# Kernel optimization log

Measured on AMD Instinct MI355X. Metric: run time of the kernel, lower is better.

## Reference

```python
import jax, jax.numpy as jnp
import numpy as np
import math

B, S, H = 2, 4096, 512
NUM_HEADS = 8
HEAD_DIM = H // NUM_HEADS
RECENCY_DECAY = 0.9


def setup_inputs() -> dict:
    key = jax.random.key(0)
    k1, k2, k3 = jax.random.split(key, 3)
    scale = 1.0 / math.sqrt(H)
    x = jax.random.normal(k1, (B, S, H), dtype=jnp.float32)
    w_qkv = jax.random.normal(k2, (3 * H, H), dtype=jnp.float32) * scale
    w_out = jax.random.normal(k3, (H, H), dtype=jnp.float32) * scale
    b_out = jnp.zeros((H,), dtype=jnp.float32)
    return {"x": x, "w_qkv": w_qkv, "w_out": w_out, "b_out": b_out}


def reference(x, w_qkv, w_out, b_out):
    batch, seq_len, hidden = x.shape
    nh, hd = NUM_HEADS, HEAD_DIM
    # qkv projection (no bias): torch Linear computes x @ W.T
    qkv = jnp.einsum('bsh,oh->bso', x, w_qkv)
    qkv = qkv.reshape(batch, seq_len, 3, nh, hd)
    q, k, v = jnp.transpose(qkv, (2, 0, 3, 1, 4))  # each [B, nh, S, hd]
    attn = jnp.einsum('bhqd,bhkd->bhqk', q, k) / math.sqrt(hd)
    # recency bias: positions[i, j] = j - i; bias = (j-i)*log(decay) for j<=i else 0
    pos = jnp.arange(seq_len)[None, :] - jnp.arange(seq_len)[:, None]
    bias = jnp.where(pos <= 0, pos.astype(jnp.float32) * math.log(RECENCY_DECAY),
                     jnp.zeros((), dtype=jnp.float32))
    attn = jax.nn.softmax(attn + bias[None, None, :, :], axis=-1)
    out = jnp.einsum('bhqk,bhkd->bqhd', attn, v).reshape(batch, seq_len, hidden)
    return jnp.einsum('bsh,oh->bso', out, w_out) + b_out
```

## Files before the change

### kernel.cpp

```cpp
#include <hip/hip_runtime.h>
#include <hip/hip_bf16.h>
#include <hip/hip_fp16.h>
#include <stdint.h>

#define B_   2
#define S_   4096
#define H_   512
#define NH_  8
#define HD_  64
#define M_   (B_*S_)
#define LOG2D (-0.15200309344504997f)
#define SC2   (0.18033688011112042f)

#define NFULL        4
#define NCHUNK       8

typedef __attribute__((ext_vector_type(8))) short bf16x8_t;
typedef __attribute__((ext_vector_type(4))) float f32x4_t;

__device__ __forceinline__ void gl_lds16(const __hip_bfloat16* g, __hip_bfloat16* l) {
  __builtin_amdgcn_global_load_lds(
      (__attribute__((address_space(1))) void*)(g),
      (__attribute__((address_space(3))) void*)(l),
      16, 0, 0);
}

__global__ __launch_bounds__(256)
void cast3_kernel(const float* __restrict__ x, const float* __restrict__ wq,
                  const float* __restrict__ wo,
                  __hip_bfloat16* __restrict__ xb, __hip_bfloat16* __restrict__ wqb,
                  __hip_bfloat16* __restrict__ wob) {
  const int N0 = M_ * H_;
  const int N1 = 3 * H_ * H_;
  int i4 = (blockIdx.x * blockDim.x + threadIdx.x) * 4;
  const float* src; __hip_bfloat16* dst; int off;
  if (i4 < N0)           { src = x;  dst = xb;  off = i4; }
  else if (i4 < N0 + N1) { src = wq; dst = wqb; off = i4 - N0; }
  else                   { src = wo; dst = wob; off = i4 - N0 - N1; }
  float4 v = *(const float4*)(src + off);
  ushort4 o;
  __hip_bfloat16 h;
  h = __float2bfloat16(v.x); o.x = *(unsigned short*)&h;
  h = __float2bfloat16(v.y); o.y = *(unsigned short*)&h;
  h = __float2bfloat16(v.z); o.z = *(unsigned short*)&h;
  h = __float2bfloat16(v.w); o.w = *(unsigned short*)&h;
  *(ushort4*)((unsigned short*)dst + off) = o;
}

template<int EPI>
__global__ __launch_bounds__(256)
void gemm_bt(const __hip_bfloat16* __restrict__ A,
             const __hip_bfloat16* __restrict__ Bw,
             int K,
             __hip_bfloat16* __restrict__ qb,
             __hip_bfloat16* __restrict__ kb,
             __hip_bfloat16* __restrict__ vtb,
             float* __restrict__ outp,
             const float* __restrict__ bias) {
  __shared__ alignas(16) __hip_bfloat16 sA[128*64];
  __shared__ alignas(16) __hip_bfloat16 sB[128*64];
  const int tid  = threadIdx.x;
  const int wave = tid >> 6, lane = tid & 63;
  const int quad = lane >> 4, l15 = lane & 15;
  const int wr = (wave >> 1) * 64, wc = (wave & 1) * 64;

  const int nbx  = gridDim.x;
  const int flat = blockIdx.y * nbx + blockIdx.x;
  const int xcd  = flat & 7, sq = flat >> 3;
  const int rows_per_xcd = gridDim.y >> 3;
  const int by = xcd * rows_per_xcd + sq / nbx;
  const int bx = sq % nbx;
  const int m0 = by * 128, n0 = bx * 128;

  const int sub  = lane >> 3;
  const int plog = (lane & 7) ^ sub;

  f32x4_t acc[4][4] = {};

  for (int kt = 0; kt < K; kt += 64) {
    __syncthreads();
    #pragma unroll
    for (int cc = 0; cc < 4; cc++) {
      int c   = wave * 4 + cc;
      int row = c * 8 + sub;
      gl_lds16(A  + (size_t)(m0 + row) * K + kt + plog * 8, sA + c * 512);
      gl_lds16(Bw + (size_t)(n0 + row) * K + kt + plog * 8, sB + c * 512);
    }
    __syncthreads();
    #pragma unroll
    for (int kh = 0; kh < 2; kh++) {
      bf16x8_t af[4], bfr[4];
      #pragma unroll
      for (int x = 0; x < 4; x++) {
        int row = wr + x * 16 + l15;
        int pos = kh * 4 + quad;
        af[x] = *(const bf16x8_t*)(sA + row * 64 + ((pos ^ (row & 7)) << 3));
      }
      #pragma unroll
      for (int y = 0; y < 4; y++) {
        int row = wc + y * 16 + l15;
        int pos = kh * 4 + quad;
        bfr[y] = *(const bf16x8_t*)(sB + row * 64 + ((pos ^ (row & 7)) << 3));
      }
      #pragma unroll
      for (int x = 0; x < 4; x++)
        #pragma unroll
        for (int y = 0; y < 4; y++)
          acc[x][y] = __builtin_amdgcn_mfma_f32_16x16x32_bf16(af[x], bfr[y], acc[x][y], 0, 0, 0);
    }
  }

  if (EPI == 0 && (n0 >> 9) == 2) {
    #pragma unroll
    for (int x = 0; x < 4; x++) {
      int gr = m0 + wr + x * 16 + quad * 4;
      int bb = gr >> 12, sb = gr & 4095;
      #pragma unroll
      for (int y = 0; y < 4; y++) {
        int rem = (n0 - 1024) + wc + y * 16 + l15;
        int h = rem >> 6, d = rem & 63;
        ushort4 o; __hip_bfloat16 hv;
        hv = __float2bfloat16(acc[x][y][0]); o.x = *(unsigned short*)&hv;
        hv = __float2bfloat16(acc[x][y][1]); o.y = *(unsigned short*)&hv;
        hv = __float2bfloat16(acc[x][y][2]); o.z = *(unsigned short*)&hv;
        hv = __float2bfloat16(acc[x][y][3]); o.w = *(unsigned short*)&hv;
        *(ushort4*)(vtb + ((size_t)(bb * NH_ + h) * HD_ + d) * S_ + sb) = o;
      }
    }
  } else {
    #pragma unroll
    for (int x = 0; x < 4; x++) {
      #pragma unroll
      for (int y = 0; y < 4; y++) {
        #pragma unroll
        for (int r = 0; r < 4; r++) {
          int gr = m0 + wr + x*16 + quad*4 + r;
          int gc = n0 + wc + y*16 + l15;
          float v = acc[x][y][r];
          if (EPI == 0) {
            int bb = gr >> 12, s = gr & 4095;
            int t  = gc >> 9,  rem = gc & 511;
            int h  = rem >> 6, d = rem & 63;
            __hip_bfloat16 hv = __float2bfloat16(v);
            int bh = bb * NH_ + h;
            if (t == 0) qb[((size_t)bh * S_ + s) * HD_ + d] = hv;
            else        kb[((size_t)bh * S_ + s) * HD_ + d] = hv;
          } else {
            outp[(size_t)gr * H_ + gc] = v + bias[gc];
          }
        }
      }
    }
  }
}

__device__ __forceinline__ void stage_kv(const __hip_bfloat16* __restrict__ kb,
                                         const __hip_bfloat16* __restrict__ vtb,
                                         int bh, int j0,
                                         __hip_bfloat16* dK, __hip_bfloat16* dV,
                                         int wave, int lane, int sub, int plog) {
  if (wave < 2) {
    #pragma unroll
    for (int cc = 0; cc < 4; cc++) {
      int c = wave * 4 + cc;
      gl_lds16(kb + ((size_t)bh * S_ + j0 + c * 8 + sub) * HD_ + plog * 8, dK + c * 512);
    }
  } else {
    #pragma unroll
    for (int cc = 0; cc < 4; cc++) {
      int c = (wave - 2) * 4 + cc;
      gl_lds16(vtb + ((size_t)bh * HD_ + c * 8 + sub) * S_ + j0 + plog * 8, dV + c * 512);
    }
  }
}

__global__ __launch_bounds__(256)
void attn_kernel(const __hip_bfloat16* __restrict__ qb,
                 const __hip_bfloat16* __restrict__ kb,
                 const __hip_bfloat16* __restrict__ vtb,
                 __hip_bfloat16* __restrict__ ob,
                 __half* __restrict__ pO,
                 float* __restrict__ pl) {
  __shared__ alignas(16) __hip_bfloat16 sK[2][64*64];
  __shared__ alignas(16) __hip_bfloat16 sV[2][64*64];
  __shared__ alignas(16) __hip_bfloat16 sP[4][16*64];

  const int tid  = threadIdx.x;
  const int wave = tid >> 6, lane = tid & 63;
  const int quad = lane >> 4, l15 = lane & 15;
  const int w  = blockIdx.x;
  const int bh = blockIdx.y;

  int q0, jt0, niter, chunk = 0;
  bool direct;
  if (w < 60) { q0 = 256 + w * 64; jt0 = 0; niter = 4; direct = true; }
  else { int t = w - 60; chunk = t & 7; q0 = (t >> 3) * 64; jt0 = chunk * 8; niter = 8; direct = false; }

  const __hip_bfloat16* qrow = qb + ((size_t)bh * S_ + q0 + wave * 16 + l15) * HD_;
  bf16x8_t aQ0 = *(const bf16x8_t*)(qrow + quad * 8);
  bf16x8_t aQ1 = *(const bf16x8_t*)(qrow + 32 + quad * 8);

  f32x4_t accO[4] = {};
  float l_r[4], negM2[4];
  const int row_i = q0 + wave * 16 + quad * 4;
  #pragma unroll
  for (int r = 0; r < 4; r++) {
    l_r[r] = 0.f;
    negM2[r] = -(17.312340f - LOG2D * (float)(row_i + r));
  }

  const int sub  = lane >> 3;
  const int plog = (lane & 7) ^ sub;
  __hip_bfloat16* sPw = &sP[wave][0];

  stage_kv(kb, vtb, bh, jt0 * 64, &sK[0][0], &sV[0][0], wave, lane, sub, plog);

  for (int it = 0; it < niter; ++it) {
    const int cur = it & 1;
    __syncthreads();
    if (it < niter - 1)
      stage_kv(kb, vtb, bh, (jt0 + it + 1) * 64,
               &sK[1 - cur][0], &sV[1 - cur][0], wave, lane, sub, plog);
    const __hip_bfloat16* cK = &sK[cur][0];
    const __hip_bfloat16* cV = &sV[cur][0];
    const int j0 = (jt0 + it) * 64;

    f32x4_t sfr[4];
    #pragma unroll
    for (int ni = 0; ni < 4; ni++) {
      int row = ni * 16 + l15;
      f32x4_t a = {};
      bf16x8_t b0 = *(const bf16x8_t*)(cK + row * 64 + ((quad       ^ (row & 7)) << 3));
      bf16x8_t b1 = *(const bf16x8_t*)(cK + row * 64 + (((quad + 4) ^ (row & 7)) << 3));
      a = __builtin_amdgcn_mfma_f32_16x16x32_bf16(aQ0, b0, a, 0, 0, 0);
      a = __builtin_amdgcn_mfma_f32_16x16x32_bf16(aQ1, b1, a, 0, 0, 0);
      sfr[ni] = a;
    }

    #pragma unroll
    for (int r = 0; r < 4; r++) {
      const float d0 = (float)(j0 + l15 - (row_i + r));
      const int row = quad * 4 + r;
      float psum = 0.f;
      #pragma unroll
      for (int ni = 0; ni < 4; ni++) {
        float dij = d0 + (float)(ni * 16);
        float arg = fmaf(fminf(dij, 0.f), LOG2D, fmaf(sfr[ni][r], SC2, negM2[r]));
        float p = __builtin_amdgcn_exp2f(arg);
        psum += p;
        int col = ni * 16 + l15;
        sPw[row * 64 + (((col >> 3) ^ (row & 7)) << 3) + (col & 7)] = __float2bfloat16(p);
      }
      l_r[r] += psum;
    }
    __builtin_amdgcn_sched_barrier(0);
    __builtin_amdgcn_s_waitcnt(0xC07F);
    __builtin_amdgcn_sched_barrier(0);

    bf16x8_t aP0 = *(const bf16x8_t*)(sPw + l15 * 64 + ((quad       ^ (l15 & 7)) << 3));
    bf16x8_t aP1 = *(const bf16x8_t*)(sPw + l15 * 64 + (((quad + 4) ^ (l15 & 7)) << 3));
    #pragma unroll
    for (int nd = 0; nd < 4; nd++) {
      int row = nd * 16 + l15;
      bf16x8_t b0 = *(const bf16x8_t*)(cV + row * 64 + ((quad       ^ (row & 7)) << 3));
      bf16x8_t b1 = *(const bf16x8_t*)(cV + row * 64 + (((quad + 4) ^ (row & 7)) << 3));
      accO[nd] = __builtin_amdgcn_mfma_f32_16x16x32_bf16(aP0, b0, accO[nd], 0, 0, 0);
      accO[nd] = __builtin_amdgcn_mfma_f32_16x16x32_bf16(aP1, b1, accO[nd], 0, 0, 0);
    }
    __builtin_amdgcn_sched_barrier(0);
  }

  #pragma unroll
  for (int r = 0; r < 4; r++) {
    float l = l_r[r];
    #pragma unroll
    for (int msk = 1; msk < 16; msk <<= 1) l += __shfl_xor(l, msk, 64);
    l_r[r] = l;
  }

  if (direct) {
    const int b = bh >> 3, h = bh & 7;
    #pragma unroll
    for (int r = 0; r < 4; r++) {
      float invr = 1.0f / l_r[r];
      #pragma unroll
      for (int nd = 0; nd < 4; nd++) {
        int srow = q0 + wave * 16 + quad * 4 + r;
        int col  = h * HD_ + nd * 16 + l15;
        ob[((size_t)b * S_ + srow) * H_ + col] = __float2bfloat16(accO[nd][r] * invr);
      }
    }
  } else {
    const int qt = q0 >> 6;
    size_t base = ((size_t)bh * NFULL + qt) * NCHUNK + chunk;
    __half* po = pO + base * 4096;
    #pragma unroll
    for (int nd = 0; nd < 4; nd++)
      #pragma unroll
      for (int r = 0; r < 4; r++)
        po[(wave*16 + quad*4 + r) * 64 + nd*16 + l15] = __float2half(accO[nd][r]);
    if (l15 == 0) {
      #pragma unroll
      for (int r = 0; r < 4; r++)
        pl[base * 64 + wave*16 + quad*4 + r] = l_r[r];
    }
  }
}

__global__ __launch_bounds__(256)
void combine_kernel(const __half* __restrict__ pO,
                    const float* __restrict__ pl,
                    __hip_bfloat16* __restrict__ ob) {
  const int f  = blockIdx.x;
  const int bh = blockIdx.y;
  const int tid = threadIdx.x;
  const int rr = tid >> 2, cg = (tid & 3) * 16;
  const size_t base0 = ((size_t)bh * NFULL + f) * NCHUNK;

  float L = 0.f;
  #pragma unroll
  for (int c = 0; c < NCHUNK; c++) L += pl[(base0 + c) * 64 + rr];
  const float inv = 1.0f / L;

  float o[16];
  #pragma unroll
  for (int k = 0; k < 16; k++) o[k] = 0.f;
  #pragma unroll
  for (int c = 0; c < NCHUNK; c++) {
    const __half* src = pO + (base0 + c) * 4096 + rr * 64 + cg;
    #pragma unroll
    for (int k = 0; k < 16; k++) o[k] += __half2float(src[k]);
  }
  const int b = bh >> 3, h = bh & 7, s = f * 64 + rr;
  __hip_bfloat16* dst = ob + ((size_t)b * S_ + s) * H_ + h * HD_ + cg;
  #pragma unroll
  for (int k = 0; k < 16; k++) dst[k] = __float2bfloat16(o[k] * inv);
}

extern "C" void kernel_launch(void* const* d_in, const int* in_sizes, int n_in,
                              void* d_out, int out_size, void* d_ws, size_t ws_size,
                              hipStream_t stream) {
  const float* x     = (const float*)d_in[0];
  const float* w_qkv = (const float*)d_in[1];
  const float* w_out = (const float*)d_in[2];
  const float* b_out = (const float*)d_in[3];
  float* out = (float*)d_out;

  char* ws = (char*)d_ws;
  __hip_bfloat16* xb  = (__hip_bfloat16*)(ws);
  __hip_bfloat16* wqb = (__hip_bfloat16*)(ws + (8u  << 20));
  __hip_bfloat16* wob = (__hip_bfloat16*)(ws + (10u << 20));
  __hip_bfloat16* qb  = (__hip_bfloat16*)(ws + (11u << 20));
  __hip_bfloat16* kb  = (__hip_bfloat16*)(ws + (19u << 20));
  __hip_bfloat16* vtb = (__hip_bfloat16*)(ws + (27u << 20));
  __half*         pO  = (__half*)(ws + (36u << 20));
  float*          pl  = (float*)(ws + (41u << 20));
  __hip_bfloat16* ab  = xb;

  cast3_kernel<<<dim3(5120), dim3(256), 0, stream>>>(x, w_qkv, w_out, xb, wqb, wob);
  gemm_bt<0><<<dim3(12, 64), dim3(256), 0, stream>>>(xb, wqb, H_, qb, kb, vtb, nullptr, nullptr);
  attn_kernel<<<dim3(60 + NFULL * NCHUNK, B_ * NH_), dim3(256), 0, stream>>>(qb, kb, vtb, ab, pO, pl);
  combine_kernel<<<dim3(NFULL, B_ * NH_), dim3(256), 0, stream>>>(pO, pl, ab);
  gemm_bt<1><<<dim3(4, 64), dim3(256), 0, stream>>>(ab, wob, H_, nullptr, nullptr, nullptr, out, b_out);
}
```

Measured before the change: 137.6 us.

## Fuse fp32-to-bf16 casts into GEMM loads and split-KV combine into output GEMM

Removes the standalone cast kernel: both GEMMs now load fp32 x and weights directly, convert to bf16 in registers and store to swizzled LDS. The combine kernel is folded into the output projection, where row blocks covering the split-KV query tiles reduce the partial fp16 outputs and normalisers on the fly while staging the A tile. This drops two launches and the bf16 intermediate round trips. In exchange the async global-to-LDS loads give way to synchronous register loads, which double global read bytes for the weights and x, and weights are re-converted by every block.

```diff
diff --git a/kernel.cpp b/kernel.cpp
--- a/kernel.cpp
+++ b/kernel.cpp
@@ -17,6 +17,7 @@
 
 typedef __attribute__((ext_vector_type(8))) short bf16x8_t;
 typedef __attribute__((ext_vector_type(4))) float f32x4_t;
+typedef __attribute__((ext_vector_type(8))) _Float16 f16x8_t;
 
 __device__ __forceinline__ void gl_lds16(const __hip_bfloat16* g, __hip_bfloat16* l) {
   __builtin_amdgcn_global_load_lds(
@@ -25,38 +26,25 @@
       16, 0, 0);
 }
 
+__device__ __forceinline__ bf16x8_t cvt8(float4 a, float4 b) {
+  bf16x8_t r; __hip_bfloat16 h;
+  h = __float2bfloat16(a.x); r[0] = *(short*)&h;
+  h = __float2bfloat16(a.y); r[1] = *(short*)&h;
+  h = __float2bfloat16(a.z); r[2] = *(short*)&h;
+  h = __float2bfloat16(a.w); r[3] = *(short*)&h;
+  h = __float2bfloat16(b.x); r[4] = *(short*)&h;
+  h = __float2bfloat16(b.y); r[5] = *(short*)&h;
+  h = __float2bfloat16(b.z); r[6] = *(short*)&h;
+  h = __float2bfloat16(b.w); r[7] = *(short*)&h;
+  return r;
+}
+
 __global__ __launch_bounds__(256)
-void cast3_kernel(const float* __restrict__ x, const float* __restrict__ wq,
-                  const float* __restrict__ wo,
-                  __hip_bfloat16* __restrict__ xb, __hip_bfloat16* __restrict__ wqb,
-                  __hip_bfloat16* __restrict__ wob) {
-  const int N0 = M_ * H_;
-  const int N1 = 3 * H_ * H_;
-  int i4 = (blockIdx.x * blockDim.x + threadIdx.x) * 4;
-  const float* src; __hip_bfloat16* dst; int off;
-  if (i4 < N0)           { src = x;  dst = xb;  off = i4; }
-  else if (i4 < N0 + N1) { src = wq; dst = wqb; off = i4 - N0; }
-  else                   { src = wo; dst = wob; off = i4 - N0 - N1; }
-  float4 v = *(const float4*)(src + off);
-  ushort4 o;
-  __hip_bfloat16 h;
-  h = __float2bfloat16(v.x); o.x = *(unsigned short*)&h;
-  h = __float2bfloat16(v.y); o.y = *(unsigned short*)&h;
-  h = __float2bfloat16(v.z); o.z = *(unsigned short*)&h;
-  h = __float2bfloat16(v.w); o.w = *(unsigned short*)&h;
-  *(ushort4*)((unsigned short*)dst + off) = o;
-}
-
-template<int EPI>
-__global__ __launch_bounds__(256)
-void gemm_bt(const __hip_bfloat16* __restrict__ A,
-             const __hip_bfloat16* __restrict__ Bw,
-             int K,
-             __hip_bfloat16* __restrict__ qb,
-             __hip_bfloat16* __restrict__ kb,
-             __hip_bfloat16* __restrict__ vtb,
-             float* __restrict__ outp,
-             const float* __restrict__ bias) {
+void gemm_qkv(const float* __restrict__ A,
+              const float* __restrict__ Bw,
+              __hip_bfloat16* __restrict__ qb,
+              __hip_bfloat16* __restrict__ kb,
+              __hip_bfloat16* __restrict__ vtb) {
   __shared__ alignas(16) __hip_bfloat16 sA[128*64];
   __shared__ alignas(16) __hip_bfloat16 sB[128*64];
   const int tid  = threadIdx.x;
@@ -77,14 +65,20 @@
 
   f32x4_t acc[4][4] = {};
 
-  for (int kt = 0; kt < K; kt += 64) {
+  for (int kt = 0; kt < H_; kt += 64) {
     __syncthreads();
     #pragma unroll
     for (int cc = 0; cc < 4; cc++) {
       int c   = wave * 4 + cc;
       int row = c * 8 + sub;
-      gl_lds16(A  + (size_t)(m0 + row) * K + kt + plog * 8, sA + c * 512);
-      gl_lds16(Bw + (size_t)(n0 + row) * K + kt + plog * 8, sB + c * 512);
+      const float* ga = A  + (size_t)(m0 + row) * H_ + kt + plog * 8;
+      const float* gb = Bw + (size_t)(n0 + row) * H_ + kt + plog * 8;
+      float4 a0 = *(const float4*)ga;
+      float4 a1 = *(const float4*)(ga + 4);
+      float4 b0 = *(const float4*)gb;
+      float4 b1 = *(const float4*)(gb + 4);
+      *(bf16x8_t*)(sA + c * 512 + lane * 8) = cvt8(a0, a1);
+      *(bf16x8_t*)(sB + c * 512 + lane * 8) = cvt8(b0, b1);
     }
     __syncthreads();
     #pragma unroll
@@ -110,7 +104,7 @@
     }
   }
 
-  if (EPI == 0 && (n0 >> 9) == 2) {
+  if ((n0 >> 9) == 2) {
     #pragma unroll
     for (int x = 0; x < 4; x++) {
       int gr = m0 + wr + x * 16 + quad * 4;
@@ -137,17 +131,13 @@
           int gr = m0 + wr + x*16 + quad*4 + r;
           int gc = n0 + wc + y*16 + l15;
           float v = acc[x][y][r];
-          if (EPI == 0) {
-            int bb = gr >> 12, s = gr & 4095;
-            int t  = gc >> 9,  rem = gc & 511;
-            int h  = rem >> 6, d = rem & 63;
-            __hip_bfloat16 hv = __float2bfloat16(v);
-            int bh = bb * NH_ + h;
-            if (t == 0) qb[((size_t)bh * S_ + s) * HD_ + d] = hv;
-            else        kb[((size_t)bh * S_ + s) * HD_ + d] = hv;
-          } else {
-            outp[(size_t)gr * H_ + gc] = v + bias[gc];
-          }
+          int bb = gr >> 12, s = gr & 4095;
+          int t  = gc >> 9,  rem = gc & 511;
+          int h  = rem >> 6, d = rem & 63;
+          __hip_bfloat16 hv = __float2bfloat16(v);
+          int bh = bb * NH_ + h;
+          if (t == 0) qb[((size_t)bh * S_ + s) * HD_ + d] = hv;
+          else        kb[((size_t)bh * S_ + s) * HD_ + d] = hv;
         }
       }
     }
@@ -308,33 +298,117 @@
 }
 
 __global__ __launch_bounds__(256)
-void combine_kernel(const __half* __restrict__ pO,
-                    const float* __restrict__ pl,
-                    __hip_bfloat16* __restrict__ ob) {
-  const int f  = blockIdx.x;
-  const int bh = blockIdx.y;
-  const int tid = threadIdx.x;
-  const int rr = tid >> 2, cg = (tid & 3) * 16;
-  const size_t base0 = ((size_t)bh * NFULL + f) * NCHUNK;
-
-  float L = 0.f;
+void gemm_out(const __hip_bfloat16* __restrict__ ab,
+              const float* __restrict__ Bw,
+              const __half* __restrict__ pO,
+              const float* __restrict__ pl,
+              float* __restrict__ outp,
+              const float* __restrict__ bias) {
+  __shared__ alignas(16) __hip_bfloat16 sA[128*64];
+  __shared__ alignas(16) __hip_bfloat16 sB[128*64];
+  const int tid  = threadIdx.x;
+  const int wave = tid >> 6, lane = tid & 63;
+  const int quad = lane >> 4, l15 = lane & 15;
+  const int wr = (wave >> 1) * 64, wc = (wave & 1) * 64;
+
+  const int nbx  = gridDim.x;
+  const int flat = blockIdx.y * nbx + blockIdx.x;
+  const int xcd  = flat & 7, sq = flat >> 3;
+  const int rows_per_xcd = gridDim.y >> 3;
+  const int by = xcd * rows_per_xcd + sq / nbx;
+  const int bx = sq % nbx;
+  const int m0 = by * 128, n0 = bx * 128;
+  const bool comb = (by & 31) < 2;
+
+  const int sub  = lane >> 3;
+  const int plog = (lane & 7) ^ sub;
+
+  f32x4_t acc[4][4] = {};
+
+  for (int kt = 0; kt < H_; kt += 64) {
+    __syncthreads();
+    if (comb) {
+      const int h  = kt >> 6;
+      const int bb = m0 >> 12;
+      const int bh = bb * NH_ + h;
+      #pragma unroll
+      for (int cc = 0; cc < 4; cc++) {
+        int c   = wave * 4 + cc;
+        int row = c * 8 + sub;
+        int s   = (m0 & 4095) + row;
+        int qt  = s >> 6, rq = s & 63;
+        size_t base0 = ((size_t)bh * NFULL + qt) * NCHUNK;
+        float L = 0.f;
+        float o[8] = {};
+        #pragma unroll
+        for (int ch = 0; ch < NCHUNK; ch++) {
+          L += pl[(base0 + ch) * 64 + rq];
+          f16x8_t v = *(const f16x8_t*)(pO + (base0 + ch) * 4096 + rq * 64 + plog * 8);
+          #pragma unroll
+          for (int k = 0; k < 8; k++) o[k] += (float)v[k];
+        }
+        float inv = 1.0f / L;
+        bf16x8_t rr;
+        #pragma unroll
+        for (int k = 0; k < 8; k++) {
+          __hip_bfloat16 hv = __float2bfloat16(o[k] * inv);
+          rr[k] = *(short*)&hv;
+        }
+        *(bf16x8_t*)(sA + c * 512 + lane * 8) = rr;
+      }
+    } else {
+      #pragma unroll
+      for (int cc = 0; cc < 4; cc++) {
+        int c   = wave * 4 + cc;
+        int row = c * 8 + sub;
+        gl_lds16(ab + (size_t)(m0 + row) * H_ + kt + plog * 8, sA + c * 512);
+      }
+    }
+    #pragma unroll
+    for (int cc = 0; cc < 4; cc++) {
+      int c   = wave * 4 + cc;
+      int row = c * 8 + sub;
+      const float* gb = Bw + (size_t)(n0 + row) * H_ + kt + plog * 8;
+      float4 b0 = *(const float4*)gb;
+      float4 b1 = *(const float4*)(gb + 4);
+      *(bf16x8_t*)(sB + c * 512 + lane * 8) = cvt8(b0, b1);
+    }
+    __syncthreads();
+    #pragma unroll
+    for (int kh = 0; kh < 2; kh++) {
+      bf16x8_t af[4], bfr[4];
+      #pragma unroll
+      for (int x = 0; x < 4; x++) {
+        int row = wr + x * 16 + l15;
+        int pos = kh * 4 + quad;
+        af[x] = *(const bf16x8_t*)(sA + row * 64 + ((pos ^ (row & 7)) << 3));
+      }
+      #pragma unroll
+      for (int y = 0; y < 4; y++) {
+        int row = wc + y * 16 + l15;
+        int pos = kh * 4 + quad;
+        bfr[y] = *(const bf16x8_t*)(sB + row * 64 + ((pos ^ (row & 7)) << 3));
+      }
+      #pragma unroll
+      for (int x = 0; x < 4; x++)
+        #pragma unroll
+        for (int y = 0; y < 4; y++)
+          acc[x][y] = __builtin_amdgcn_mfma_f32_16x16x32_bf16(af[x], bfr[y], acc[x][y], 0, 0, 0);
+    }
+  }
+
   #pragma unroll
-  for (int c = 0; c < NCHUNK; c++) L += pl[(base0 + c) * 64 + rr];
-  const float inv = 1.0f / L;
-
-  float o[16];
-  #pragma unroll
-  for (int k = 0; k < 16; k++) o[k] = 0.f;
-  #pragma unroll
-  for (int c = 0; c < NCHUNK; c++) {
-    const __half* src = pO + (base0 + c) * 4096 + rr * 64 + cg;
-    #pragma unroll
-    for (int k = 0; k < 16; k++) o[k] += __half2float(src[k]);
-  }
-  const int b = bh >> 3, h = bh & 7, s = f * 64 + rr;
-  __hip_bfloat16* dst = ob + ((size_t)b * S_ + s) * H_ + h * HD_ + cg;
-  #pragma unroll
-  for (int k = 0; k < 16; k++) dst[k] = __float2bfloat16(o[k] * inv);
+  for (int x = 0; x < 4; x++) {
+    #pragma unroll
+    for (int y = 0; y < 4; y++) {
+      #pragma unroll
+      for (int r = 0; r < 4; r++) {
+        int gr = m0 + wr + x*16 + quad*4 + r;
+        int gc = n0 + wc + y*16 + l15;
+        outp[(size_t)gr * H_ + gc] = acc[x][y][r] + bias[gc];
+      }
+    }
+  }
 }
 
 extern "C" void kernel_launch(void* const* d_in, const int* in_sizes, int n_in,
@@ -347,19 +421,14 @@
   float* out = (float*)d_out;
 
   char* ws = (char*)d_ws;
-  __hip_bfloat16* xb  = (__hip_bfloat16*)(ws);
-  __hip_bfloat16* wqb = (__hip_bfloat16*)(ws + (8u  << 20));
-  __hip_bfloat16* wob = (__hip_bfloat16*)(ws + (10u << 20));
-  __hip_bfloat16* qb  = (__hip_bfloat16*)(ws + (11u << 20));
-  __hip_bfloat16* kb  = (__hip_bfloat16*)(ws + (19u << 20));
-  __hip_bfloat16* vtb = (__hip_bfloat16*)(ws + (27u << 20));
-  __half*         pO  = (__half*)(ws + (36u << 20));
-  float*          pl  = (float*)(ws + (41u << 20));
-  __hip_bfloat16* ab  = xb;
-
-  cast3_kernel<<<dim3(5120), dim3(256), 0, stream>>>(x, w_qkv, w_out, xb, wqb, wob);
-  gemm_bt<0><<<dim3(12, 64), dim3(256), 0, stream>>>(xb, wqb, H_, qb, kb, vtb, nullptr, nullptr);
+  __hip_bfloat16* ab  = (__hip_bfloat16*)(ws);
+  __hip_bfloat16* qb  = (__hip_bfloat16*)(ws + (8u  << 20));
+  __hip_bfloat16* kb  = (__hip_bfloat16*)(ws + (16u << 20));
+  __hip_bfloat16* vtb = (__hip_bfloat16*)(ws + (24u << 20));
+  __half*         pO  = (__half*)(ws + (32u << 20));
+  float*          pl  = (float*)(ws + (36u << 20));
+
+  gemm_qkv<<<dim3(12, 64), dim3(256), 0, stream>>>(x, w_qkv, qb, kb, vtb);
   attn_kernel<<<dim3(60 + NFULL * NCHUNK, B_ * NH_), dim3(256), 0, stream>>>(qb, kb, vtb, ab, pO, pl);
-  combine_kernel<<<dim3(NFULL, B_ * NH_), dim3(256), 0, stream>>>(pO, pl, ab);
-  gemm_bt<1><<<dim3(4, 64), dim3(256), 0, stream>>>(ab, wob, H_, nullptr, nullptr, nullptr, out, b_out);
-}
+  gemm_out<<<dim3(4, 64), dim3(256), 0, stream>>>(ab, w_out, pO, pl, out, b_out);
+}
```

New measurement: 164.4 us. 1.2x slower.
